# Optimization experiments

Hardware: AMD Instinct MI355X
Metric: run time of the kernel (lower is better)

Reference implementation:

```python
import jax, jax.numpy as jnp
import numpy as np

C = 512
B, H, W = 8, 64, 64
GROUPS = 32
EPS = 1e-6


def setup_inputs() -> dict:
    key = jax.random.key(0)
    ks = jax.random.split(key, 6)
    s = 1.0 / np.sqrt(C)
    return {
        "x": jax.random.normal(ks[0], (B, C, H, W), dtype=jnp.float32),
        "gn_scale": jnp.ones((C,), jnp.float32),
        "gn_bias": jnp.zeros((C,), jnp.float32),
        "wq": jax.random.normal(ks[1], (C, C), jnp.float32) * s,
        "bq": jnp.zeros((C,), jnp.float32),
        "wk": jax.random.normal(ks[2], (C, C), jnp.float32) * s,
        "bk": jnp.zeros((C,), jnp.float32),
        "wv": jax.random.normal(ks[3], (C, C), jnp.float32) * s,
        "bv": jnp.zeros((C,), jnp.float32),
        "wo": jax.random.normal(ks[4], (C, C), jnp.float32) * s,
        "bo": jnp.zeros((C,), jnp.float32),
    }


def group_norm(x, scale, bias):
    # x: [b, c, h, w]; GroupNorm(32 groups, eps=1e-6, affine)
    b, c, h, w = x.shape
    xg = x.reshape(b, GROUPS, c // GROUPS, h, w)
    mean = xg.mean(axis=(2, 3, 4), keepdims=True)
    var = xg.var(axis=(2, 3, 4), keepdims=True)
    xg = (xg - mean) * jax.lax.rsqrt(var + EPS)
    return xg.reshape(b, c, h, w) * scale[None, :, None, None] + bias[None, :, None, None]


def reference(x, gn_scale, gn_bias, wq, bq, wk, bk, wv, bv, wo, bo):
    b, c, h, w = x.shape
    n = h * w
    hn = group_norm(x, gn_scale, gn_bias).reshape(b, c, n)  # [b,c,n]
    # 1x1 convs == channel matmuls
    q = jnp.einsum('oc,bcn->bon', wq, hn) + bq[None, :, None]
    k = jnp.einsum('oc,bcn->bon', wk, hn) + bk[None, :, None]
    v = jnp.einsum('oc,bcn->bon', wv, hn) + bv[None, :, None]
    # scores: [b, n_query, n_key], softmax over keys
    scores = jnp.einsum('bcn,bcm->bnm', q, k) * (float(c) ** -0.5)
    attn = jax.nn.softmax(scores, axis=2)
    # out[b,c,i] = sum_j v[b,c,j] * attn[b,i,j]
    out = jnp.einsum('bcm,bnm->bcn', v, attn)
    out = jnp.einsum('oc,bcn->bon', wo, out) + bo[None, :, None]
    return x + out.reshape(b, c, h, w)
```

## Files before the change

kernel.cpp:

```cpp
#include <hip/hip_runtime.h>
#include <hip/hip_bf16.h>


typedef __bf16 bf16_t;
typedef __bf16 bf16x8 __attribute__((ext_vector_type(8)));
typedef __bf16 bf16x4 __attribute__((ext_vector_type(4)));
typedef float  f32x4  __attribute__((ext_vector_type(4)));

#define CDIM 512
#define NSP  4096
#define L2E  1.4426950408889634f

typedef __attribute__((address_space(1))) const void* as1_cvp;
typedef __attribute__((address_space(3))) void*       as3_vp;

__device__ __forceinline__ void gload_lds16(const void* g, void* l) {
  __builtin_amdgcn_global_load_lds((as1_cvp)g, (as3_vp)l, 16, 0, 0);
}

__global__ __launch_bounds__(256) void f32_to_bf16_k(const float* __restrict__ in,
                                                     bf16_t* __restrict__ out, int n) {
  int i = (blockIdx.x * 256 + threadIdx.x) * 4;
  if (i < n) {
    float4 v = *(const float4*)(in + i);
    bf16x4 o;
    o[0] = (bf16_t)v.x; o[1] = (bf16_t)v.y; o[2] = (bf16_t)v.z; o[3] = (bf16_t)v.w;
    *(bf16x4*)(out + i) = o;
  }
}

__global__ __launch_bounds__(256) void gn_stats_k(const float* __restrict__ x,
                                                  float* __restrict__ stats) {
  const int gid = blockIdx.x;
  const float4* base = (const float4*)(x + (long)gid * 65536);
  float s = 0.f, ss = 0.f;
  for (int i = threadIdx.x; i < 16384; i += 256) {
    float4 t = base[i];
    s  += t.x + t.y + t.z + t.w;
    ss += t.x*t.x + t.y*t.y + t.z*t.z + t.w*t.w;
  }
#pragma unroll
  for (int o = 32; o; o >>= 1) { s += __shfl_xor(s, o); ss += __shfl_xor(ss, o); }
  __shared__ float rs[4], rss[4];
  const int lane = threadIdx.x & 63, wid = threadIdx.x >> 6;
  if (lane == 0) { rs[wid] = s; rss[wid] = ss; }
  __syncthreads();
  if (threadIdx.x == 0) {
    s  = rs[0] + rs[1] + rs[2] + rs[3];
    ss = rss[0] + rss[1] + rss[2] + rss[3];
    float mean = s * (1.f / 65536.f);
    float var  = ss * (1.f / 65536.f) - mean * mean;
    stats[gid]       = mean;
    stats[256 + gid] = rsqrtf(var + 1e-6f);
  }
}

__global__ __launch_bounds__(256) void gn_apply_k(const float* __restrict__ x,
                                                  const float* __restrict__ stats,
                                                  const float* __restrict__ gw,
                                                  const float* __restrict__ gb,
                                                  bf16_t* __restrict__ hnT) {
  __shared__ float tile[64 * 65];
  const int n0 = blockIdx.x * 64;
  const int c0 = blockIdx.y * 64;
  const int b  = blockIdx.z;
  const int tid = threadIdx.x;
  {
    const int cl = tid >> 2, nq = tid & 3;
    const int c = c0 + cl;
    const int g = c >> 4;
    const float mean = stats[b * 32 + g];
    const float rstd = stats[256 + b * 32 + g];
    const float a  = rstd * gw[c];
    const float bb = gb[c] - mean * a;
    const float4* xr = (const float4*)(x + ((long)b * CDIM + c) * NSP + n0 + nq * 16);
#pragma unroll
    for (int i = 0; i < 4; i++) {
      float4 t = xr[i];
      float* d = &tile[cl * 65 + nq * 16 + i * 4];
      d[0] = t.x * a + bb; d[1] = t.y * a + bb; d[2] = t.z * a + bb; d[3] = t.w * a + bb;
    }
  }
  __syncthreads();
  {
    const int nl = tid >> 2, cq = tid & 3;
    union { bf16_t h[16]; uint4 v[2]; } o;
#pragma unroll
    for (int j = 0; j < 16; j++) o.h[j] = (bf16_t)tile[(cq * 16 + j) * 65 + nl];
    bf16_t* dst = hnT + ((long)b * NSP + n0 + nl) * CDIM + c0 + cq * 16;
    ((uint4*)dst)[0] = o.v[0];
    ((uint4*)dst)[1] = o.v[1];
  }
}

template <int MODE>
__global__ __launch_bounds__(256) void gemm_bt_k(
    const bf16_t* __restrict__ A, long sAb, long ldA,
    const bf16_t* __restrict__ B, long sBb, long ldB,
    void* __restrict__ Cout, long sCb, long ldC, void* __restrict__ Cout2,
    int M, int N, int K,
    const float* __restrict__ bias_row,
    const float* __restrict__ bias_col,
    float scale,
    const float* __restrict__ residual, long sRb) {
  __shared__ __align__(16) bf16_t sA[128 * 32];
  __shared__ __align__(16) bf16_t sB[128 * 32];

  const int tid  = threadIdx.x;
  const int lane = tid & 63;
  const int wid  = tid >> 6;
  const int wm = wid >> 1, wn = wid & 1;
  const int b = blockIdx.z;
  const int rowBase = blockIdx.y * 128;
  const int colBase = blockIdx.x * 128;

  const bf16_t* Ab = A + (long)b * sAb + (long)rowBase * ldA;
  const bf16_t* Bb = B + (long)b * sBb + (long)colBase * ldB;

  f32x4 acc[4][4];
#pragma unroll
  for (int i = 0; i < 4; i++)
#pragma unroll
    for (int j = 0; j < 4; j++) acc[i][j] = (f32x4){0.f, 0.f, 0.f, 0.f};

  const int q0 = tid, q1 = tid + 256;
  const int r0 = q0 >> 2, k0c = (q0 & 3) * 8;
  const int r1 = q1 >> 2, k1c = (q1 & 3) * 8;
  const int mrow  = lane & 15;
  const int kfrag = (lane >> 4) * 8;

  for (int kt = 0; kt < K; kt += 32) {
    gload_lds16(Ab + (long)r0 * ldA + kt + k0c, sA + q0 * 8);
    gload_lds16(Ab + (long)r1 * ldA + kt + k1c, sA + q1 * 8);
    gload_lds16(Bb + (long)r0 * ldB + kt + k0c, sB + q0 * 8);
    gload_lds16(Bb + (long)r1 * ldB + kt + k1c, sB + q1 * 8);
    __syncthreads();
    bf16x8 af[4], bfr[4];
#pragma unroll
    for (int t = 0; t < 4; t++) {
      af[t]  = *(const bf16x8*)&sA[(wm * 64 + t * 16 + mrow) * 32 + kfrag];
      bfr[t] = *(const bf16x8*)&sB[(wn * 64 + t * 16 + mrow) * 32 + kfrag];
    }
#pragma unroll
    for (int i = 0; i < 4; i++)
#pragma unroll
      for (int j = 0; j < 4; j++)
        acc[i][j] = __builtin_amdgcn_mfma_f32_16x16x32_bf16(af[i], bfr[j], acc[i][j], 0, 0, 0);
    __syncthreads();
  }

  const int quad = lane >> 4;
  const int colf = lane & 15;
#pragma unroll
  for (int i = 0; i < 4; i++) {
#pragma unroll
    for (int j = 0; j < 4; j++) {
#pragma unroll
      for (int r = 0; r < 4; r++) {
        const int row = rowBase + wm * 64 + i * 16 + quad * 4 + r;
        const int col = colBase + wn * 64 + j * 16 + colf;
        float v = acc[i][j][r];
        if (MODE == 2) {
          if (col < 512)
            ((bf16_t*)Cout)[(long)b * sCb + (long)row * ldC + col] =
                (bf16_t)((v + bias_col[col]) * scale);
          else
            ((bf16_t*)Cout2)[(long)b * sCb + (long)row * ldC + (col - 512)] =
                (bf16_t)(v + bias_row[col - 512]);
        } else {
          if (bias_row) v += bias_row[row];
          if (bias_col) v += bias_col[col];
          v *= scale;
          if (residual) v += residual[(long)b * sRb + (long)row * ldC + col];
          if (MODE == 1)
            ((bf16_t*)Cout)[(long)b * sCb + (long)row * ldC + col] = (bf16_t)v;
          else
            ((float*)Cout)[(long)b * sCb + (long)row * ldC + col] = v;
        }
      }
    }
  }
}

__global__ __launch_bounds__(256, 2) void flash_attn_k(
    const bf16_t* __restrict__ QT, const bf16_t* __restrict__ KT,
    const bf16_t* __restrict__ V, bf16_t* __restrict__ O1T) {
  __shared__ __align__(16) bf16_t sK[64 * 520];
  __shared__ __align__(16) bf16_t sP[4][16 * 72];

  const int tid = threadIdx.x, lane = tid & 63, w = tid >> 6;
  const int quad = lane >> 4, l15 = lane & 15;
  const int b = blockIdx.y, q0 = blockIdx.x * 64;

  const bf16_t* Qw = QT + ((long)b * NSP + q0 + w * 16) * CDIM;
  const bf16_t* Kb = KT + (long)b * NSP * CDIM;
  const bf16_t* Vb = V  + (long)b * NSP * CDIM;

  bf16x8 qf[16];
#pragma unroll
  for (int kc = 0; kc < 16; kc++)
    qf[kc] = *(const bf16x8*)(Qw + (long)l15 * CDIM + kc * 32 + quad * 8);

  f32x4 oacc[32];
#pragma unroll
  for (int i = 0; i < 32; i++) oacc[i] = (f32x4){0.f, 0.f, 0.f, 0.f};
  float m_r[4] = {-3e38f, -3e38f, -3e38f, -3e38f};
  float l_r[4] = {0.f, 0.f, 0.f, 0.f};

  for (int j0 = 0; j0 < NSP; j0 += 64) {
    __syncthreads();
#pragma unroll
    for (int i = 0; i < 16; i++) {
      const int key = w * 16 + i;
      gload_lds16(Kb + (long)(j0 + key) * CDIM + lane * 8, sK + key * 520 + lane * 8);
    }
    __syncthreads();

    f32x4 sacc[4];
#pragma unroll
    for (int t = 0; t < 4; t++) sacc[t] = (f32x4){0.f, 0.f, 0.f, 0.f};
#pragma unroll
    for (int kc = 0; kc < 16; kc++) {
#pragma unroll
      for (int t = 0; t < 4; t++) {
        bf16x8 kf = *(const bf16x8*)(sK + (t * 16 + l15) * 520 + kc * 32 + quad * 8);
        sacc[t] = __builtin_amdgcn_mfma_f32_16x16x32_bf16(qf[kc], kf, sacc[t], 0, 0, 0);
      }
    }

    float alpha[4];
#pragma unroll
    for (int r = 0; r < 4; r++) {
      float mx = fmaxf(fmaxf(sacc[0][r], sacc[1][r]), fmaxf(sacc[2][r], sacc[3][r]));
      mx = fmaxf(mx, __shfl_xor(mx, 1));
      mx = fmaxf(mx, __shfl_xor(mx, 2));
      mx = fmaxf(mx, __shfl_xor(mx, 4));
      mx = fmaxf(mx, __shfl_xor(mx, 8));
      const float mn = fmaxf(m_r[r], mx);
      alpha[r] = exp2f((m_r[r] - mn) * L2E);
      m_r[r] = mn;
      float rs = 0.f;
#pragma unroll
      for (int t = 0; t < 4; t++) {
        const float p = exp2f((sacc[t][r] - mn) * L2E);
        sacc[t][r] = p;
        rs += p;
      }
      rs += __shfl_xor(rs, 1); rs += __shfl_xor(rs, 2);
      rs += __shfl_xor(rs, 4); rs += __shfl_xor(rs, 8);
      l_r[r] = l_r[r] * alpha[r] + rs;
    }
    const f32x4 av = {alpha[0], alpha[1], alpha[2], alpha[3]};
#pragma unroll
    for (int i = 0; i < 32; i++) oacc[i] *= av;

#pragma unroll
    for (int t = 0; t < 4; t++)
#pragma unroll
      for (int r = 0; r < 4; r++)
        sP[w][(quad * 4 + r) * 72 + t * 16 + l15] = (bf16_t)sacc[t][r];
    const bf16x8 pf0 = *(const bf16x8*)(&sP[w][l15 * 72 + quad * 8]);
    const bf16x8 pf1 = *(const bf16x8*)(&sP[w][l15 * 72 + 32 + quad * 8]);

#pragma unroll
    for (int h = 0; h < 2; h++) {
      __syncthreads();
      uint4 tv[8];
#pragma unroll
      for (int i = 0; i < 8; i++) {
        const int g = i * 256 + tid, c = g >> 3, off = g & 7;
        tv[i] = *(const uint4*)(Vb + (long)(h * 256 + c) * NSP + j0 + off * 8);
      }
#pragma unroll
      for (int i = 0; i < 8; i++) {
        const int g = i * 256 + tid, c = g >> 3, off = g & 7;
        *(uint4*)(sK + c * 72 + off * 8) = tv[i];
      }
      __syncthreads();
#pragma unroll
      for (int ct = 0; ct < 16; ct++) {
        const bf16x8 vf0 = *(const bf16x8*)(sK + (ct * 16 + l15) * 72 + quad * 8);
        const bf16x8 vf1 = *(const bf16x8*)(sK + (ct * 16 + l15) * 72 + 32 + quad * 8);
        oacc[h * 16 + ct] =
            __builtin_amdgcn_mfma_f32_16x16x32_bf16(pf0, vf0, oacc[h * 16 + ct], 0, 0, 0);
        oacc[h * 16 + ct] =
            __builtin_amdgcn_mfma_f32_16x16x32_bf16(pf1, vf1, oacc[h * 16 + ct], 0, 0, 0);
      }
    }
  }

  const f32x4 linv = {1.f / l_r[0], 1.f / l_r[1], 1.f / l_r[2], 1.f / l_r[3]};
  __syncthreads();
#pragma unroll
  for (int ct = 0; ct < 32; ct++) {
    const f32x4 o = oacc[ct] * linv;
#pragma unroll
    for (int r = 0; r < 4; r++)
      sK[(w * 16 + quad * 4 + r) * 520 + ct * 16 + l15] = (bf16_t)o[r];
  }
  __syncthreads();
  bf16_t* Ob = O1T + ((long)b * NSP + q0) * CDIM;
#pragma unroll
  for (int i = 0; i < 16; i++) {
    const int g = i * 256 + tid, row = g >> 6, off = g & 63;
    *(uint4*)(Ob + (long)row * CDIM + off * 8) = *(const uint4*)(sK + row * 520 + off * 8);
  }
}

extern "C" void kernel_launch(void* const* d_in, const int* in_sizes, int n_in,
                              void* d_out, int out_size, void* d_ws, size_t ws_size,
                              hipStream_t stream) {
  const float* x        = (const float*)d_in[0];
  const float* gn_scale = (const float*)d_in[1];
  const float* gn_bias  = (const float*)d_in[2];
  const float* wq = (const float*)d_in[3];
  const float* bq = (const float*)d_in[4];
  const float* wk = (const float*)d_in[5];
  const float* bk = (const float*)d_in[6];
  const float* wv = (const float*)d_in[7];
  const float* bv = (const float*)d_in[8];
  const float* wo = (const float*)d_in[9];
  const float* bo = (const float*)d_in[10];
  float* out = (float*)d_out;

  const long PB = 2097152;
  const long MB = 1048576L;
  char* w = (char*)d_ws;
  bf16_t* hnT  = (bf16_t*)(w);
  bf16_t* O1T  = hnT;
  bf16_t* QT   = (bf16_t*)(w + 32 * MB);
  bf16_t* KT   = (bf16_t*)(w + 64 * MB);
  bf16_t* V    = (bf16_t*)(w + 96 * MB);
  bf16_t* wqkb = (bf16_t*)(w + 128 * MB);
  bf16_t* wvb  = (bf16_t*)(w + 129 * MB);
  bf16_t* wob  = (bf16_t*)(w + 129 * MB + 524288L);
  float*  stats = (float*)(w + 130 * MB);

  const float qscale = 0.044194173824159216f;

  f32_to_bf16_k<<<256, 256, 0, stream>>>(wq, wqkb, 262144);
  f32_to_bf16_k<<<256, 256, 0, stream>>>(wk, wqkb + 262144, 262144);
  f32_to_bf16_k<<<256, 256, 0, stream>>>(wv, wvb, 262144);
  f32_to_bf16_k<<<256, 256, 0, stream>>>(wo, wob, 262144);

  gn_stats_k<<<256, 256, 0, stream>>>(x, stats);
  gn_apply_k<<<dim3(64, 8, 8), 256, 0, stream>>>(x, stats, gn_scale, gn_bias, hnT);

  gemm_bt_k<2><<<dim3(8, 32, 8), 256, 0, stream>>>(
      hnT, PB, 512, wqkb, 0, 512, QT, PB, 512, KT, 4096, 1024, 512,
      bk, bq, qscale, nullptr, 0);
  gemm_bt_k<1><<<dim3(32, 4, 8), 256, 0, stream>>>(
      wvb, 0, 512, hnT, PB, 512, V, PB, 4096, nullptr, 512, 4096, 512,
      bv, nullptr, 1.f, nullptr, 0);

  flash_attn_k<<<dim3(64, 8), 256, 0, stream>>>(QT, KT, V, O1T);

  gemm_bt_k<0><<<dim3(32, 4, 8), 256, 0, stream>>>(
      wob, 0, 512, O1T, PB, 512, (void*)out, PB, 4096, nullptr, 512, 4096, 512,
      bo, nullptr, 1.f, x, PB);
}
```

Before: 1.154 ms.

## Double-buffer K/V staging with async LDS loads and XOR swizzle in flash attention

Restructures the flash attention loop into four phases over two 32 KB LDS buffers. Each phase issues async global-to-LDS loads for the next K or V half while MFMAs run on the current one, with vmcnt-based waits and raw barriers. V is now loaded directly to LDS via global_load_lds instead of through registers, and both K and V use an XOR swizzle in place of padding to avoid bank conflicts. It also raises wave priority around MFMA sections and flattens the grid so batch varies fastest, so consecutive blocks cover different batches. The hand-written waitcnt and barrier sequencing adds correctness risk.

```diff
diff --git a/kernel.cpp b/kernel.cpp
--- a/kernel.cpp
+++ b/kernel.cpp
@@ -182,20 +182,56 @@
   }
 }
 
+__device__ __forceinline__ void stage_k(const bf16_t* __restrict__ Kb, int j0, int h,
+                                        bf16_t* dst, int tid) {
+#pragma unroll
+  for (int i = 0; i < 8; ++i) {
+    const int e = i * 2048 + tid * 8;
+    const int row = e >> 8;
+    const int slot = (e >> 3) & 31;
+    gload_lds16(Kb + (long)(j0 + row) * CDIM + h * 256 + ((slot ^ (row & 7)) << 3),
+                dst + e);
+  }
+}
+
+__device__ __forceinline__ void stage_v(const bf16_t* __restrict__ Vb, int j0, int h,
+                                        bf16_t* dst, int tid) {
+#pragma unroll
+  for (int i = 0; i < 8; ++i) {
+    const int e = i * 2048 + tid * 8;
+    const int row = e >> 6;
+    const int slot = (e >> 3) & 7;
+    gload_lds16(Vb + (long)(h * 256 + row) * NSP + j0 + ((slot ^ (row & 7)) << 3),
+                dst + e);
+  }
+}
+
+#define PH_WAIT8() do { asm volatile("s_waitcnt vmcnt(8)\n\ts_barrier" ::: "memory"); \
+                        __builtin_amdgcn_sched_barrier(0); } while (0)
+#define PH_WAIT0() do { asm volatile("s_waitcnt vmcnt(0)\n\ts_barrier" ::: "memory"); \
+                        __builtin_amdgcn_sched_barrier(0); } while (0)
+#define PH_END()   do { asm volatile("s_barrier" ::: "memory"); \
+                        __builtin_amdgcn_sched_barrier(0); } while (0)
+
 __global__ __launch_bounds__(256, 2) void flash_attn_k(
     const bf16_t* __restrict__ QT, const bf16_t* __restrict__ KT,
     const bf16_t* __restrict__ V, bf16_t* __restrict__ O1T) {
-  __shared__ __align__(16) bf16_t sK[64 * 520];
+  __shared__ __align__(16) bf16_t sBuf[2][16384];
   __shared__ __align__(16) bf16_t sP[4][16 * 72];
 
   const int tid = threadIdx.x, lane = tid & 63, w = tid >> 6;
   const int quad = lane >> 4, l15 = lane & 15;
-  const int b = blockIdx.y, q0 = blockIdx.x * 64;
+  const int sw = l15 & 7;
+  const int bid = blockIdx.x;
+  const int b = bid & 7;
+  const int q0 = (bid >> 3) * 64;
 
   const bf16_t* Qw = QT + ((long)b * NSP + q0 + w * 16) * CDIM;
   const bf16_t* Kb = KT + (long)b * NSP * CDIM;
   const bf16_t* Vb = V  + (long)b * NSP * CDIM;
 
+  stage_k(Kb, 0, 0, &sBuf[0][0], tid);
+
   bf16x8 qf[16];
 #pragma unroll
   for (int kc = 0; kc < 16; kc++)
@@ -207,103 +243,128 @@
   float m_r[4] = {-3e38f, -3e38f, -3e38f, -3e38f};
   float l_r[4] = {0.f, 0.f, 0.f, 0.f};
 
-  for (int j0 = 0; j0 < NSP; j0 += 64) {
-    __syncthreads();
-#pragma unroll
-    for (int i = 0; i < 16; i++) {
-      const int key = w * 16 + i;
-      gload_lds16(Kb + (long)(j0 + key) * CDIM + lane * 8, sK + key * 520 + lane * 8);
-    }
-    __syncthreads();
-
+#pragma unroll 1
+  for (int it = 0; it < 64; ++it) {
+    const int j0 = it * 64;
     f32x4 sacc[4];
 #pragma unroll
     for (int t = 0; t < 4; t++) sacc[t] = (f32x4){0.f, 0.f, 0.f, 0.f};
-#pragma unroll
-    for (int kc = 0; kc < 16; kc++) {
+    bf16x8 pf0, pf1;
+
+    stage_k(Kb, j0, 1, &sBuf[1][0], tid);
+    PH_WAIT8();
+    __builtin_amdgcn_s_setprio(1);
+#pragma unroll
+    for (int kc = 0; kc < 8; kc++) {
 #pragma unroll
       for (int t = 0; t < 4; t++) {
-        bf16x8 kf = *(const bf16x8*)(sK + (t * 16 + l15) * 520 + kc * 32 + quad * 8);
+        const bf16x8 kf = *(const bf16x8*)(
+            &sBuf[0][(t * 16 + l15) * 256 + (((kc * 4 + quad) ^ sw) << 3)]);
         sacc[t] = __builtin_amdgcn_mfma_f32_16x16x32_bf16(qf[kc], kf, sacc[t], 0, 0, 0);
       }
     }
-
-    float alpha[4];
-#pragma unroll
-    for (int r = 0; r < 4; r++) {
-      float mx = fmaxf(fmaxf(sacc[0][r], sacc[1][r]), fmaxf(sacc[2][r], sacc[3][r]));
-      mx = fmaxf(mx, __shfl_xor(mx, 1));
-      mx = fmaxf(mx, __shfl_xor(mx, 2));
-      mx = fmaxf(mx, __shfl_xor(mx, 4));
-      mx = fmaxf(mx, __shfl_xor(mx, 8));
-      const float mn = fmaxf(m_r[r], mx);
-      alpha[r] = exp2f((m_r[r] - mn) * L2E);
-      m_r[r] = mn;
-      float rs = 0.f;
+    __builtin_amdgcn_s_setprio(0);
+    PH_END();
+
+    stage_v(Vb, j0, 0, &sBuf[0][0], tid);
+    PH_WAIT8();
+    __builtin_amdgcn_s_setprio(1);
+#pragma unroll
+    for (int kc = 8; kc < 16; kc++) {
 #pragma unroll
       for (int t = 0; t < 4; t++) {
-        const float p = exp2f((sacc[t][r] - mn) * L2E);
-        sacc[t][r] = p;
-        rs += p;
+        const bf16x8 kf = *(const bf16x8*)(
+            &sBuf[1][(t * 16 + l15) * 256 + ((((kc - 8) * 4 + quad) ^ sw) << 3)]);
+        sacc[t] = __builtin_amdgcn_mfma_f32_16x16x32_bf16(qf[kc], kf, sacc[t], 0, 0, 0);
       }
-      rs += __shfl_xor(rs, 1); rs += __shfl_xor(rs, 2);
-      rs += __shfl_xor(rs, 4); rs += __shfl_xor(rs, 8);
-      l_r[r] = l_r[r] * alpha[r] + rs;
-    }
-    const f32x4 av = {alpha[0], alpha[1], alpha[2], alpha[3]};
-#pragma unroll
-    for (int i = 0; i < 32; i++) oacc[i] *= av;
+    }
+    __builtin_amdgcn_s_setprio(0);
+
+    {
+      float alpha[4];
+#pragma unroll
+      for (int r = 0; r < 4; r++) {
+        float mx = fmaxf(fmaxf(sacc[0][r], sacc[1][r]), fmaxf(sacc[2][r], sacc[3][r]));
+        mx = fmaxf(mx, __shfl_xor(mx, 1));
+        mx = fmaxf(mx, __shfl_xor(mx, 2));
+        mx = fmaxf(mx, __shfl_xor(mx, 4));
+        mx = fmaxf(mx, __shfl_xor(mx, 8));
+        const float mn = fmaxf(m_r[r], mx);
+        alpha[r] = exp2f((m_r[r] - mn) * L2E);
+        m_r[r] = mn;
+        float rs = 0.f;
+#pragma unroll
+        for (int t = 0; t < 4; t++) {
+          const float p = exp2f((sacc[t][r] - mn) * L2E);
+          sacc[t][r] = p;
+          rs += p;
+        }
+        rs += __shfl_xor(rs, 1); rs += __shfl_xor(rs, 2);
+        rs += __shfl_xor(rs, 4); rs += __shfl_xor(rs, 8);
+        l_r[r] = l_r[r] * alpha[r] + rs;
+      }
+      const f32x4 av = {alpha[0], alpha[1], alpha[2], alpha[3]};
+#pragma unroll
+      for (int i = 0; i < 32; i++) oacc[i] *= av;
+    }
 
 #pragma unroll
     for (int t = 0; t < 4; t++)
 #pragma unroll
       for (int r = 0; r < 4; r++)
         sP[w][(quad * 4 + r) * 72 + t * 16 + l15] = (bf16_t)sacc[t][r];
-    const bf16x8 pf0 = *(const bf16x8*)(&sP[w][l15 * 72 + quad * 8]);
-    const bf16x8 pf1 = *(const bf16x8*)(&sP[w][l15 * 72 + 32 + quad * 8]);
-
-#pragma unroll
-    for (int h = 0; h < 2; h++) {
-      __syncthreads();
-      uint4 tv[8];
-#pragma unroll
-      for (int i = 0; i < 8; i++) {
-        const int g = i * 256 + tid, c = g >> 3, off = g & 7;
-        tv[i] = *(const uint4*)(Vb + (long)(h * 256 + c) * NSP + j0 + off * 8);
-      }
-#pragma unroll
-      for (int i = 0; i < 8; i++) {
-        const int g = i * 256 + tid, c = g >> 3, off = g & 7;
-        *(uint4*)(sK + c * 72 + off * 8) = tv[i];
-      }
-      __syncthreads();
-#pragma unroll
-      for (int ct = 0; ct < 16; ct++) {
-        const bf16x8 vf0 = *(const bf16x8*)(sK + (ct * 16 + l15) * 72 + quad * 8);
-        const bf16x8 vf1 = *(const bf16x8*)(sK + (ct * 16 + l15) * 72 + 32 + quad * 8);
-        oacc[h * 16 + ct] =
-            __builtin_amdgcn_mfma_f32_16x16x32_bf16(pf0, vf0, oacc[h * 16 + ct], 0, 0, 0);
-        oacc[h * 16 + ct] =
-            __builtin_amdgcn_mfma_f32_16x16x32_bf16(pf1, vf1, oacc[h * 16 + ct], 0, 0, 0);
-      }
-    }
+    pf0 = *(const bf16x8*)(&sP[w][l15 * 72 + quad * 8]);
+    pf1 = *(const bf16x8*)(&sP[w][l15 * 72 + 32 + quad * 8]);
+    PH_END();
+
+    stage_v(Vb, j0, 1, &sBuf[1][0], tid);
+    PH_WAIT8();
+    __builtin_amdgcn_s_setprio(1);
+#pragma unroll
+    for (int ct = 0; ct < 16; ct++) {
+      const int row = ct * 16 + l15;
+      const bf16x8 vf0 = *(const bf16x8*)(&sBuf[0][row * 64 + ((quad ^ sw) << 3)]);
+      const bf16x8 vf1 = *(const bf16x8*)(&sBuf[0][row * 64 + (((4 + quad) ^ sw) << 3)]);
+      oacc[ct] = __builtin_amdgcn_mfma_f32_16x16x32_bf16(pf0, vf0, oacc[ct], 0, 0, 0);
+      oacc[ct] = __builtin_amdgcn_mfma_f32_16x16x32_bf16(pf1, vf1, oacc[ct], 0, 0, 0);
+    }
+    __builtin_amdgcn_s_setprio(0);
+    PH_END();
+
+    if (it < 63) {
+      stage_k(Kb, j0 + 64, 0, &sBuf[0][0], tid);
+      PH_WAIT8();
+    } else {
+      PH_WAIT0();
+    }
+    __builtin_amdgcn_s_setprio(1);
+#pragma unroll
+    for (int ct = 0; ct < 16; ct++) {
+      const int row = ct * 16 + l15;
+      const bf16x8 vf0 = *(const bf16x8*)(&sBuf[1][row * 64 + ((quad ^ sw) << 3)]);
+      const bf16x8 vf1 = *(const bf16x8*)(&sBuf[1][row * 64 + (((4 + quad) ^ sw) << 3)]);
+      oacc[16 + ct] = __builtin_amdgcn_mfma_f32_16x16x32_bf16(pf0, vf0, oacc[16 + ct], 0, 0, 0);
+      oacc[16 + ct] = __builtin_amdgcn_mfma_f32_16x16x32_bf16(pf1, vf1, oacc[16 + ct], 0, 0, 0);
+    }
+    __builtin_amdgcn_s_setprio(0);
+    PH_END();
   }
 
   const f32x4 linv = {1.f / l_r[0], 1.f / l_r[1], 1.f / l_r[2], 1.f / l_r[3]};
-  __syncthreads();
+  bf16_t* sO = &sBuf[0][0];
 #pragma unroll
   for (int ct = 0; ct < 32; ct++) {
     const f32x4 o = oacc[ct] * linv;
 #pragma unroll
     for (int r = 0; r < 4; r++)
-      sK[(w * 16 + quad * 4 + r) * 520 + ct * 16 + l15] = (bf16_t)o[r];
+      sO[(w * 16 + quad * 4 + r) * 512 + ct * 16 + l15] = (bf16_t)o[r];
   }
   __syncthreads();
   bf16_t* Ob = O1T + ((long)b * NSP + q0) * CDIM;
 #pragma unroll
   for (int i = 0; i < 16; i++) {
     const int g = i * 256 + tid, row = g >> 6, off = g & 63;
-    *(uint4*)(Ob + (long)row * CDIM + off * 8) = *(const uint4*)(sK + row * 520 + off * 8);
+    *(uint4*)(Ob + (long)row * CDIM + off * 8) = *(const uint4*)(sO + row * 512 + off * 8);
   }
 }
 
@@ -353,7 +414,7 @@
       wvb, 0, 512, hnT, PB, 512, V, PB, 4096, nullptr, 512, 4096, 512,
       bv, nullptr, 1.f, nullptr, 0);
 
-  flash_attn_k<<<dim3(64, 8), 256, 0, stream>>>(QT, KT, V, O1T);
+  flash_attn_k<<<dim3(512), 256, 0, stream>>>(QT, KT, V, O1T);
 
   gemm_bt_k<0><<<dim3(32, 4, 8), 256, 0, stream>>>(
       wob, 0, 512, O1T, PB, 512, (void*)out, PB, 4096, nullptr, 512, 4096, 512,
```

New measurement: 1.141 ms. No clear change (-1.1%).
